# Kernel tuning notes

Measured on AMD Instinct MI355X. Metric: run time of the kernel, lower is better.

## Reference

```python
import jax, jax.numpy as jnp
import numpy as np

B, E, S, D, F = 8, 8, 8192, 64, 256  # batch, local_num_experts, seq, d_model, dim_feedforward

def setup_inputs() -> dict:
    key = jax.random.key(0)
    k1, k2, k3 = jax.random.split(key, 3)
    x = jax.random.normal(k1, (B, E, S, D), dtype=jnp.float32)
    # kaiming-uniform-ish scale for the per-expert weights
    bound1 = 1.0 / np.sqrt(D)
    bound2 = 1.0 / np.sqrt(F)
    weight1 = jax.random.uniform(k2, (E, D, F), dtype=jnp.float32, minval=-bound1, maxval=bound1)
    weight2 = jax.random.uniform(k3, (E, F, D), dtype=jnp.float32, minval=-bound2, maxval=bound2)
    return {"x": x, "weight1": weight1, "weight2": weight2}

def reference(x, weight1, weight2):
    # Faithful to torch: x.reshape(E, -1, d_model) reinterprets contiguous memory,
    # grouping B*S tokens per expert slot; then batched GEMM -> relu -> batched GEMM.
    input_shape = x.shape
    d_model = input_shape[-1]
    n_exp = weight1.shape[0]
    xr = x.reshape(n_exp, -1, d_model)              # [E, T, D], T = B*S
    h = jax.nn.relu(jnp.einsum('etd,edf->etf', xr, weight1))  # [E, T, F]
    out = jnp.einsum('etf,efd->etd', h, weight2)    # [E, T, D]
    return out.reshape(input_shape)
```

## Files before the change

### kernel.cpp

```cpp
#include <hip/hip_runtime.h>
#include <hip/hip_bf16.h>

typedef __attribute__((ext_vector_type(8))) short short8;
typedef __attribute__((ext_vector_type(16))) float f32x16;

__device__ __forceinline__ unsigned short bfbits(float f) {
  return __builtin_bit_cast(unsigned short, __float2bfloat16(f));
}

__device__ __forceinline__ short8 lds_read16(const short* p, int byteOff) {
  return *reinterpret_cast<const short8*>(reinterpret_cast<const char*>(p) + byteOff);
}

#define MFMA(a, b, c) __builtin_amdgcn_mfma_f32_32x32x16_bf16((a), (b), (c), 0, 0, 0)

__launch_bounds__(512, 2)
__global__ void ffn_fused(const float* __restrict__ x,
                          const float* __restrict__ w1,
                          const float* __restrict__ w2,
                          float* __restrict__ out) {
  __shared__ short w1t[4 * 2 * 256 * 8];
  __shared__ short w2t[16 * 2 * 64 * 8];

  const int tid  = threadIdx.x;
  const int lane = tid & 63;
  const int wv   = tid >> 6;
  const int m    = lane & 31;
  const int g    = lane >> 5;

  const int e     = blockIdx.x & 7;
  const int chunk = blockIdx.x >> 3;

  const float* W1 = w1 + e * (64 * 256);
  const float* W2 = w2 + e * (256 * 64);

  const long rowBase = (long)e * 65536 + (long)chunk * 1024 + wv * 128;

  {
    const int f  = tid & 255;
    const int cb = (tid >> 8) * 4;
#pragma unroll 2
    for (int ci = 0; ci < 4; ++ci) {
      const int c  = cb + ci;
      const int d0 = c * 8;
      unsigned w0, w1v, w2v, w3;
      {
        float a0 = W1[(d0 + 0) * 256 + f], a1 = W1[(d0 + 1) * 256 + f];
        float a2 = W1[(d0 + 2) * 256 + f], a3 = W1[(d0 + 3) * 256 + f];
        float a4 = W1[(d0 + 4) * 256 + f], a5 = W1[(d0 + 5) * 256 + f];
        float a6 = W1[(d0 + 6) * 256 + f], a7 = W1[(d0 + 7) * 256 + f];
        w0 = (unsigned)bfbits(a0) | ((unsigned)bfbits(a1) << 16);
        w1v = (unsigned)bfbits(a2) | ((unsigned)bfbits(a3) << 16);
        w2v = (unsigned)bfbits(a4) | ((unsigned)bfbits(a5) << 16);
        w3 = (unsigned)bfbits(a6) | ((unsigned)bfbits(a7) << 16);
      }
      *reinterpret_cast<uint4*>(reinterpret_cast<char*>(w1t) + c * 4096 + f * 16) =
          make_uint4(w0, w1v, w2v, w3);
    }
  }
  {
    const int d = tid & 63;
    const int r = tid >> 6;
#pragma unroll 2
    for (int ci = 0; ci < 4; ++ci) {
      const int c2 = r + ci * 8;
      const int f0 = c2 * 8;
      unsigned w0, w1v, w2v, w3;
      {
        float a0 = W2[(f0 + 0) * 64 + d], a1 = W2[(f0 + 1) * 64 + d];
        float a2 = W2[(f0 + 2) * 64 + d], a3 = W2[(f0 + 3) * 64 + d];
        float a4 = W2[(f0 + 4) * 64 + d], a5 = W2[(f0 + 5) * 64 + d];
        float a6 = W2[(f0 + 6) * 64 + d], a7 = W2[(f0 + 7) * 64 + d];
        w0 = (unsigned)bfbits(a0) | ((unsigned)bfbits(a1) << 16);
        w1v = (unsigned)bfbits(a2) | ((unsigned)bfbits(a3) << 16);
        w2v = (unsigned)bfbits(a4) | ((unsigned)bfbits(a5) << 16);
        w3 = (unsigned)bfbits(a6) | ((unsigned)bfbits(a7) << 16);
      }
      *reinterpret_cast<uint4*>(reinterpret_cast<char*>(w2t) + c2 * 1024 + d * 16) =
          make_uint4(w0, w1v, w2v, w3);
    }
  }
  __syncthreads();

  const int baseA = g * 4096 + m * 16;
  const int baseW = g * 1024 + m * 16;

#pragma unroll 1
  for (int it = 0; it < 4; ++it) {
    const long rb = rowBase + it * 32;

    short8 xf[4];
#pragma unroll
    for (int ks = 0; ks < 4; ++ks) {
      const float* px = x + (rb + m) * 64 + ks * 16 + g * 8;
      const float4 u0 = *reinterpret_cast<const float4*>(px);
      const float4 u1 = *reinterpret_cast<const float4*>(px + 4);
      short8 v;
      v[0] = (short)bfbits(u0.x); v[1] = (short)bfbits(u0.y);
      v[2] = (short)bfbits(u0.z); v[3] = (short)bfbits(u0.w);
      v[4] = (short)bfbits(u1.x); v[5] = (short)bfbits(u1.y);
      v[6] = (short)bfbits(u1.z); v[7] = (short)bfbits(u1.w);
      xf[ks] = v;
    }

    f32x16 o0, o1;
#pragma unroll
    for (int i = 0; i < 16; ++i) { o0[i] = 0.f; o1[i] = 0.f; }

#pragma unroll 1
    for (int ft = 0; ft < 8; ++ft) {
      short8 a[4];
#pragma unroll
      for (int ks = 0; ks < 4; ++ks)
        a[ks] = lds_read16(w1t, baseA + ks * 8192 + ft * 512);

      f32x16 h;
#pragma unroll
      for (int i = 0; i < 16; ++i) h[i] = 0.f;
#pragma unroll
      for (int ks = 0; ks < 4; ++ks) h = MFMA(a[ks], xf[ks], h);

      unsigned pk[8];
#pragma unroll
      for (int q = 0; q < 4; ++q) {
        pk[2*q]   = (unsigned)bfbits(fmaxf(h[4*q+0], 0.f)) | ((unsigned)bfbits(fmaxf(h[4*q+1], 0.f)) << 16);
        pk[2*q+1] = (unsigned)bfbits(fmaxf(h[4*q+2], 0.f)) | ((unsigned)bfbits(fmaxf(h[4*q+3], 0.f)) << 16);
      }

#pragma unroll
      for (int sub = 0; sub < 2; ++sub) {
        const int ks2 = 2 * ft + sub;
        const short8 wA = lds_read16(w2t, baseW + ks2 * 2048);
        const short8 wB = lds_read16(w2t, baseW + 512 + ks2 * 2048);
        const int qa = 2 * sub, qb = 2 * sub + 1;

        union { short8 v; unsigned u[4]; } b;
        {
          unsigned pa0 = pk[2*qa], pa1 = pk[2*qa+1];
          unsigned pb0 = pk[2*qb], pb1 = pk[2*qb+1];
          unsigned s0 = g ? pa0 : pb0, s1 = g ? pa1 : pb1;
          unsigned k0 = g ? pb0 : pa0, k1 = g ? pb1 : pa1;
          unsigned r0 = __shfl_xor(s0, 32, 64);
          unsigned r1 = __shfl_xor(s1, 32, 64);
          b.u[0] = g ? r0 : k0; b.u[1] = g ? r1 : k1;
          b.u[2] = g ? k0 : r0; b.u[3] = g ? k1 : r1;
        }

        o0 = MFMA(wA, b.v, o0);
        o1 = MFMA(wB, b.v, o1);
      }
    }

#pragma unroll
    for (int dt = 0; dt < 2; ++dt) {
      const f32x16& acc = dt == 0 ? o0 : o1;
      float* po = out + (rb + m) * 64 + dt * 32 + g * 4;
#pragma unroll
      for (int q = 0; q < 4; ++q) {
        float4 s;
        s.x = acc[4*q+0]; s.y = acc[4*q+1]; s.z = acc[4*q+2]; s.w = acc[4*q+3];
        *reinterpret_cast<float4*>(po + 8 * q) = s;
      }
    }
  }
}

extern "C" void kernel_launch(void* const* d_in, const int* in_sizes, int n_in,
                              void* d_out, int out_size, void* d_ws, size_t ws_size,
                              hipStream_t stream) {
  const float* x  = (const float*)d_in[0];
  const float* w1 = (const float*)d_in[1];
  const float* w2 = (const float*)d_in[2];
  float* out = (float*)d_out;
  ffn_fused<<<dim3(512), dim3(512), 0, stream>>>(x, w1, w2, out);
}
```

Before: 68.13 us.

## Use 768-thread blocks with 12 waves and a smaller grid to amortize weight staging

Blocks grow from 8 to 12 waves and the grid shrinks from 512 to 344 blocks, so each block covers 1536 rows instead of 1024. The W2 staging loop is redistributed across the 12 waves with a bounds guard, W1 staging is limited to the first 512 threads, and waves whose rows fall past the end return early. The aim is to convert and stage each expert's weights into LDS less often relative to compute and to better fill the CUs. The cost is a ragged last block with idle waves, plus a different occupancy and register budget under the new launch bounds.

```diff
diff --git a/kernel.cpp b/kernel.cpp
--- a/kernel.cpp
+++ b/kernel.cpp
@@ -14,7 +14,7 @@
 
 #define MFMA(a, b, c) __builtin_amdgcn_mfma_f32_32x32x16_bf16((a), (b), (c), 0, 0, 0)
 
-__launch_bounds__(512, 2)
+__launch_bounds__(768, 2)
 __global__ void ffn_fused(const float* __restrict__ x,
                           const float* __restrict__ w1,
                           const float* __restrict__ w2,
@@ -34,53 +34,58 @@
   const float* W1 = w1 + e * (64 * 256);
   const float* W2 = w2 + e * (256 * 64);
 
-  const long rowBase = (long)e * 65536 + (long)chunk * 1024 + wv * 128;
-
-  {
+  if (tid < 512) {
     const int f  = tid & 255;
     const int cb = (tid >> 8) * 4;
 #pragma unroll 2
     for (int ci = 0; ci < 4; ++ci) {
       const int c  = cb + ci;
       const int d0 = c * 8;
-      unsigned w0, w1v, w2v, w3;
+      unsigned u0, u1, u2, u3;
       {
         float a0 = W1[(d0 + 0) * 256 + f], a1 = W1[(d0 + 1) * 256 + f];
         float a2 = W1[(d0 + 2) * 256 + f], a3 = W1[(d0 + 3) * 256 + f];
         float a4 = W1[(d0 + 4) * 256 + f], a5 = W1[(d0 + 5) * 256 + f];
         float a6 = W1[(d0 + 6) * 256 + f], a7 = W1[(d0 + 7) * 256 + f];
-        w0 = (unsigned)bfbits(a0) | ((unsigned)bfbits(a1) << 16);
-        w1v = (unsigned)bfbits(a2) | ((unsigned)bfbits(a3) << 16);
-        w2v = (unsigned)bfbits(a4) | ((unsigned)bfbits(a5) << 16);
-        w3 = (unsigned)bfbits(a6) | ((unsigned)bfbits(a7) << 16);
+        u0 = (unsigned)bfbits(a0) | ((unsigned)bfbits(a1) << 16);
+        u1 = (unsigned)bfbits(a2) | ((unsigned)bfbits(a3) << 16);
+        u2 = (unsigned)bfbits(a4) | ((unsigned)bfbits(a5) << 16);
+        u3 = (unsigned)bfbits(a6) | ((unsigned)bfbits(a7) << 16);
       }
       *reinterpret_cast<uint4*>(reinterpret_cast<char*>(w1t) + c * 4096 + f * 16) =
-          make_uint4(w0, w1v, w2v, w3);
+          make_uint4(u0, u1, u2, u3);
     }
   }
   {
     const int d = tid & 63;
     const int r = tid >> 6;
-#pragma unroll 2
-    for (int ci = 0; ci < 4; ++ci) {
-      const int c2 = r + ci * 8;
-      const int f0 = c2 * 8;
-      unsigned w0, w1v, w2v, w3;
-      {
-        float a0 = W2[(f0 + 0) * 64 + d], a1 = W2[(f0 + 1) * 64 + d];
-        float a2 = W2[(f0 + 2) * 64 + d], a3 = W2[(f0 + 3) * 64 + d];
-        float a4 = W2[(f0 + 4) * 64 + d], a5 = W2[(f0 + 5) * 64 + d];
-        float a6 = W2[(f0 + 6) * 64 + d], a7 = W2[(f0 + 7) * 64 + d];
-        w0 = (unsigned)bfbits(a0) | ((unsigned)bfbits(a1) << 16);
-        w1v = (unsigned)bfbits(a2) | ((unsigned)bfbits(a3) << 16);
-        w2v = (unsigned)bfbits(a4) | ((unsigned)bfbits(a5) << 16);
-        w3 = (unsigned)bfbits(a6) | ((unsigned)bfbits(a7) << 16);
+#pragma unroll 1
+    for (int ci = 0; ci < 3; ++ci) {
+      const int c2 = r + 12 * ci;
+      if (c2 < 32) {
+        const int f0 = c2 * 8;
+        unsigned u0, u1, u2, u3;
+        {
+          float a0 = W2[(f0 + 0) * 64 + d], a1 = W2[(f0 + 1) * 64 + d];
+          float a2 = W2[(f0 + 2) * 64 + d], a3 = W2[(f0 + 3) * 64 + d];
+          float a4 = W2[(f0 + 4) * 64 + d], a5 = W2[(f0 + 5) * 64 + d];
+          float a6 = W2[(f0 + 6) * 64 + d], a7 = W2[(f0 + 7) * 64 + d];
+          u0 = (unsigned)bfbits(a0) | ((unsigned)bfbits(a1) << 16);
+          u1 = (unsigned)bfbits(a2) | ((unsigned)bfbits(a3) << 16);
+          u2 = (unsigned)bfbits(a4) | ((unsigned)bfbits(a5) << 16);
+          u3 = (unsigned)bfbits(a6) | ((unsigned)bfbits(a7) << 16);
+        }
+        *reinterpret_cast<uint4*>(reinterpret_cast<char*>(w2t) + c2 * 1024 + d * 16) =
+            make_uint4(u0, u1, u2, u3);
       }
-      *reinterpret_cast<uint4*>(reinterpret_cast<char*>(w2t) + c2 * 1024 + d * 16) =
-          make_uint4(w0, w1v, w2v, w3);
     }
   }
   __syncthreads();
+
+  const int localBase = chunk * 1536 + wv * 128;
+  if (localBase >= 65536) return;
+
+  const long rowBase = (long)e * 65536 + localBase;
 
   const int baseA = g * 4096 + m * 16;
   const int baseW = g * 1024 + m * 16;
@@ -172,5 +177,5 @@
   const float* w1 = (const float*)d_in[1];
   const float* w2 = (const float*)d_in[2];
   float* out = (float*)d_out;
-  ffn_fused<<<dim3(512), dim3(512), 0, stream>>>(x, w1, w2, out);
+  ffn_fused<<<dim3(344), dim3(768), 0, stream>>>(x, w1, w2, out);
 }
```

Measured after the change: 78.77 us. +15.6%, slower.
